# Kernel tuning notes

Measured on AMD Instinct MI355X. Metric: run time of the kernel, lower is better.

The kernel has to match this reference:

```python
import jax, jax.numpy as jnp
import numpy as np

B, S, H = 1, 2048, 2048
NH, NKV, HD = 32, 8, 64
RBS, ICS, RBN = 64, 64, 16          # retrieval_block_size, input_chunk_size, retrieval_block_num
RLEN = RBS * RBN                     # 1024 retrieval tokens
KV = RLEN + S                        # 3072 total kv length
START = RLEN                         # INPUT_START_IDX
SCALE = HD ** -0.5
NEG = -1e9


def _document_ids():
    # mirrors get_document_ids
    ids = np.full(KV, -1, np.int32)
    ids[:START] = np.arange(START) // RBS + 1            # retrieval blocks -> 1..RBN
    chunk = np.arange(S) // ICS
    ids[START:] = np.where(chunk == 0, -1, np.minimum(chunk, RBN))
    return ids


def _block_mask():
    # mirrors causal_retrieval_mask_mod, precomputed dense [S, KV]
    ids = _document_ids()
    qpos = np.arange(S) + START
    kv = np.arange(KV)
    causal = (qpos[:, None] >= kv[None, :]) & (kv[None, :] > START)
    doc = (ids[qpos][:, None] == ids[None, :]) & (kv[None, :] < START)
    return jnp.asarray(causal | doc)


_MASK = _block_mask()


def _rotate_half(x):
    h = x.shape[-1] // 2
    return jnp.concatenate([-x[..., h:], x[..., :h]], axis=-1)


def setup_inputs() -> dict:
    key = jax.random.key(0)
    ks = jax.random.split(key, 6)
    inv_freq = 1.0 / (10000.0 ** (np.arange(0, HD, 2, dtype=np.float32) / HD))
    ang = np.arange(S, dtype=np.float32)[:, None] * inv_freq[None, :]   # [S, HD/2]
    emb = np.concatenate([ang, ang], axis=-1)                            # [S, HD]
    cos = jnp.asarray(np.cos(emb))[None].astype(jnp.float32)            # [1, S, HD]
    sin = jnp.asarray(np.sin(emb))[None].astype(jnp.float32)
    return {
        "hidden_states": jax.random.normal(ks[0], (B, S, H), jnp.float32),
        "cos": cos,
        "sin": sin,
        "retrieval_key": jax.random.normal(ks[1], (B, NKV, RLEN, HD), jnp.float32),
        "retrieval_value": jax.random.normal(ks[2], (B, NKV, RLEN, HD), jnp.float32),
        "Wq": jax.random.normal(ks[3], (H, NH * HD), jnp.float32) * 0.02,
        "Wk": jax.random.normal(ks[4], (H, NKV * HD), jnp.float32) * 0.02,
        "Wv": jax.random.normal(ks[5], (H, NKV * HD), jnp.float32) * 0.02,
        "Wo": jax.random.normal(jax.random.fold_in(key, 7), (NH * HD, H), jnp.float32) * 0.02,
    }


def reference(hidden_states, cos, sin, retrieval_key, retrieval_value, Wq, Wk, Wv, Wo):
    # QKV projections -> [B, nheads, S, HD]
    q = (hidden_states @ Wq).reshape(B, S, NH, HD).transpose(0, 2, 1, 3)
    k = (hidden_states @ Wk).reshape(B, S, NKV, HD).transpose(0, 2, 1, 3)
    v = (hidden_states @ Wv).reshape(B, S, NKV, HD).transpose(0, 2, 1, 3)
    # RoPE (retrieval kv is pre-encoded; rope only on current tokens)
    c, s = cos[:, None, :, :], sin[:, None, :, :]
    q = q * c + _rotate_half(q) * s
    k = k * c + _rotate_half(k) * s
    # prepend retrieval kv
    k = jnp.concatenate([retrieval_key, k], axis=2)    # [B, NKV, KV, HD]
    v = jnp.concatenate([retrieval_value, v], axis=2)
    # GQA: expand kv heads
    g = NH // NKV
    k = jnp.repeat(k, g, axis=1)                        # [B, NH, KV, HD]
    v = jnp.repeat(v, g, axis=1)
    scores = jnp.einsum("bhqd,bhkd->bhqk", q, k) * SCALE
    scores = jnp.where(_MASK[None, None], scores, NEG)
    probs = jax.nn.softmax(scores, axis=-1)
    # fully-masked rows (q_idx 0) -> zero output, matching flex_attention
    row_valid = _MASK.any(axis=-1)[None, None, :, None]
    probs = jnp.where(row_valid, probs, 0.0)
    out = jnp.einsum("bhqk,bhkd->bhqd", probs, v)
    out = out.transpose(0, 2, 1, 3).reshape(B, S, NH * HD)
    return out @ Wo
```

## Files before the change

kernel.cpp:

```cpp
#include <hip/hip_runtime.h>

#define S_LEN 2048
#define H_DIM 2048
#define NH 32
#define NKV 8
#define HD 64
#define RLEN 1024
#define KVTOT 3072
#define SCALE 0.125f
#define QS 0.18033688011112042f
#define FIX8 11.541560327111707f

typedef unsigned short ushort_t;
using short8 = __attribute__((ext_vector_type(8))) short;
using f32x4 = __attribute__((ext_vector_type(4))) float;

__device__ __forceinline__ float b2f(unsigned short u) {
    union { unsigned int i; float f; } v;
    v.i = ((unsigned int)u) << 16;
    return v.f;
}
__device__ __forceinline__ unsigned short f2b(float f) {
    union { float f; unsigned int i; } v;
    v.f = f;
    unsigned int x = v.i;
    return (unsigned short)((x + 0x7fffu + ((x >> 16) & 1u)) >> 16);
}

__device__ __forceinline__ void gload16(const ushort_t* g, ushort_t* l) {
    __builtin_amdgcn_global_load_lds(
        (const __attribute__((address_space(1))) unsigned int*)g,
        (__attribute__((address_space(3))) unsigned int*)l, 16, 0, 0);
}

__device__ __forceinline__ int is_f32(const void* p) {
    const unsigned int* w = (const unsigned int*)p;
    const int lane = threadIdx.x & 63;
    int cnt = 0;
#pragma unroll
    for (int j = 0; j < 4; ++j) {
        unsigned int lo = w[lane + j * 64] & 0xFFFFu;
        unsigned int e = (lo >> 7) & 0xFFu;
        cnt += (lo != 0u && (e < 90u || e > 140u)) ? 1 : 0;
    }
    unsigned long long b = __ballot(cnt >= 2);
    return __popcll(b) > 16;
}

__global__ __launch_bounds__(256) void prep_all(
    const void* __restrict__ rk, const void* __restrict__ rv,
    const void* __restrict__ Wq, const void* __restrict__ Wk,
    const void* __restrict__ Wv, const void* __restrict__ Wo,
    ushort_t* __restrict__ WqkvT, ushort_t* __restrict__ WoT,
    ushort_t* __restrict__ ktall, ushort_t* __restrict__ vtall)
{
    __shared__ ushort_t S[64 * 72];
    const int id = blockIdx.x;
    if (id < 2560) {
        int z, t;
        if (id < 1024)      { z = 0; t = id; }
        else if (id < 1280) { z = 1; t = id - 1024; }
        else if (id < 1536) { z = 2; t = id - 1280; }
        else                { z = 3; t = id - 1536; }
        const void* src = (z == 0) ? Wq : (z == 1) ? Wk : (z == 2) ? Wv : Wo;
        const int F = is_f32(src);
        const int C = (z == 1 || z == 2) ? 512 : 2048;
        const int nx = (z == 1 || z == 2) ? 8 : 32;
        const int x = t % nx, y = t / nx;
        ushort_t* dst = (z == 3) ? WoT : WqkvT;
        const int rofs = (z == 1) ? 2048 : (z == 2) ? 2560 : 0;

        const int r0 = y * 64, c0 = x * 64;
        const int lr = threadIdx.x >> 2, lc = (threadIdx.x & 3) * 16;
        ushort_t tt[16];
        if (F) {
            const float* p = (const float*)src + (size_t)(r0 + lr) * C + c0 + lc;
#pragma unroll
            for (int j = 0; j < 16; j += 4) {
                float4 f = *(const float4*)(p + j);
                tt[j] = f2b(f.x); tt[j + 1] = f2b(f.y); tt[j + 2] = f2b(f.z); tt[j + 3] = f2b(f.w);
            }
        } else {
            const ushort_t* p = (const ushort_t*)src + (size_t)(r0 + lr) * C + c0 + lc;
            *(uint4*)tt = ((const uint4*)p)[0];
            *(uint4*)(tt + 8) = ((const uint4*)p)[1];
        }
        *(uint4*)&S[lr * 72 + lc] = *(const uint4*)tt;
        *(uint4*)&S[lr * 72 + lc + 8] = *(const uint4*)(tt + 8);
        __syncthreads();
        const int wc = threadIdx.x >> 2, wr = (threadIdx.x & 3) * 16;
        ushort_t o[16];
#pragma unroll
        for (int j = 0; j < 16; ++j) o[j] = S[(wr + j) * 72 + wc];
        ushort_t* q = dst + (size_t)(rofs + c0 + wc) * 2048 + r0 + wr;
        *(uint4*)q = *(const uint4*)o;
        *(uint4*)(q + 8) = *(const uint4*)(o + 8);
    } else if (id < 2816) {
        const int kF = is_f32(rk);
        const int e = ((id - 2560) * 256 + threadIdx.x) * 8;
        const int kvh = e >> 16;
        const int rem = e & 65535;
        ushort_t* dst = ktall + (size_t)kvh * (KVTOT * 64) + rem;
        if (kF) {
            const float* p = (const float*)rk + e;
            float4 f0 = ((const float4*)p)[0];
            float4 f1 = ((const float4*)p)[1];
            ushort_t o[8];
            o[0] = f2b(f0.x); o[1] = f2b(f0.y); o[2] = f2b(f0.z); o[3] = f2b(f0.w);
            o[4] = f2b(f1.x); o[5] = f2b(f1.y); o[6] = f2b(f1.z); o[7] = f2b(f1.w);
            *(uint4*)dst = *(const uint4*)o;
        } else {
            *(uint4*)dst = *(const uint4*)((const ushort_t*)rk + e);
        }
    } else {
        const int idv = id - 2816;
        const int t = idv & 15;
        const int kvh = idv >> 4;
        const int vF = is_f32(rv);
        const int lr = threadIdx.x >> 2, lc = (threadIdx.x & 3) * 16;
        ushort_t tt[16];
        size_t base = ((size_t)kvh * RLEN + t * 64 + lr) * HD + lc;
        if (vF) {
            const float* p = (const float*)rv + base;
#pragma unroll
            for (int j = 0; j < 16; j += 4) {
                float4 f = *(const float4*)(p + j);
                tt[j] = f2b(f.x); tt[j + 1] = f2b(f.y); tt[j + 2] = f2b(f.z); tt[j + 3] = f2b(f.w);
            }
        } else {
            const ushort_t* p = (const ushort_t*)rv + base;
            *(uint4*)tt = ((const uint4*)p)[0];
            *(uint4*)(tt + 8) = ((const uint4*)p)[1];
        }
        *(uint4*)&S[lr * 72 + lc] = *(const uint4*)tt;
        *(uint4*)&S[lr * 72 + lc + 8] = *(const uint4*)(tt + 8);
        __syncthreads();
        const int wc = threadIdx.x >> 2, wr = (threadIdx.x & 3) * 16;
        ushort_t o[16];
#pragma unroll
        for (int j = 0; j < 16; ++j) o[j] = S[(wr + j) * 72 + wc];
        const int blk = t * 2 + (wr >> 5);
        ushort_t* q = vtall + (((size_t)(kvh * 96 + blk) * 64 + wc) * 32) + (wr & 31);
        *(uint4*)q = *(const uint4*)o;
        *(uint4*)(q + 8) = *(const uint4*)(o + 8);
    }
}

__global__ __launch_bounds__(256, 4) void gemm_qkv(
    const void* __restrict__ hs, const ushort_t* __restrict__ Bt,
    ushort_t* __restrict__ qkvp, ushort_t* __restrict__ ktall,
    ushort_t* __restrict__ vtall,
    const void* __restrict__ cosv, const void* __restrict__ sinv)
{
    const int K = 2048;
    const int aF = is_f32(hs);
    __shared__ __align__(16) ushort_t As[2][64 * 32];
    __shared__ __align__(16) ushort_t Bs[2][128 * 32];
    const int tid = threadIdx.x;
    const int wave = tid >> 6, lane = tid & 63;
    const int lq = lane & 15, quad = lane >> 4;
    const int m0 = blockIdx.y * 64, n0 = blockIdx.x * 128;
    const int wm = (wave & 1) * 32, wn = (wave >> 1) * 64;
    const int nk = K >> 5;

    const int ar = tid >> 2, ag = tid & 3;
    const int aslot = (ag ^ ((ar >> 1) & 3)) * 8;
    const float*    apf = (const float*)hs    + (size_t)(m0 + ar) * K + ag * 8;
    const ushort_t* aph = (const ushort_t*)hs + (size_t)(m0 + ar) * K + ag * 8;
    const int srow = wave * 16 + (lane >> 2);
    const int scol = ((lane & 3) ^ ((lane >> 3) & 3)) * 8;
    const ushort_t* gb0 = Bt + (size_t)(n0 + srow) * K + scol;
    const ushort_t* gb1 = Bt + (size_t)(n0 + 64 + srow) * K + scol;
    ushort_t* lB = &Bs[0][0] + wave * 16 * 32;
    const int rs = (lq >> 1) & 3;

    float4 af0, af1;
    uint2 au0, au1;

#define ALOAD(kt) do { \
        if (aF) { af0 = *(const float4*)(apf + (size_t)(kt) * 32); \
                  af1 = *(const float4*)(apf + (size_t)(kt) * 32 + 4); } \
        else    { au0 = *(const uint2*)(aph + (size_t)(kt) * 32); \
                  au1 = *(const uint2*)(aph + (size_t)(kt) * 32 + 4); } \
    } while (0)
#define AWRITE(buf) do { \
        ushort_t t8[8]; \
        if (aF) { t8[0]=f2b(af0.x); t8[1]=f2b(af0.y); t8[2]=f2b(af0.z); t8[3]=f2b(af0.w); \
                  t8[4]=f2b(af1.x); t8[5]=f2b(af1.y); t8[6]=f2b(af1.z); t8[7]=f2b(af1.w); } \
        else    { *(uint2*)t8 = au0; *(uint2*)(t8 + 4) = au1; } \
        *(uint4*)&As[buf][ar * 32 + aslot] = *(const uint4*)t8; \
    } while (0)
#define GLOADB(buf, kt) do { \
        gload16(gb0 + (size_t)(kt) * 32, lB + (buf) * (128 * 32)); \
        gload16(gb1 + (size_t)(kt) * 32, lB + (buf) * (128 * 32) + 64 * 32); \
    } while (0)

    f32x4 acc[2][4];
#pragma unroll
    for (int i = 0; i < 2; ++i)
#pragma unroll
        for (int j = 0; j < 4; ++j) acc[i][j] = (f32x4){0.f, 0.f, 0.f, 0.f};

    ALOAD(0); AWRITE(0);
    GLOADB(0, 0);
    int cur = 0;
    for (int kt = 0; kt < nk; ++kt) {
        const bool more = (kt + 1 < nk);
        if (more) {
            ALOAD(kt + 1);
            GLOADB(cur ^ 1, kt + 1);
            asm volatile("s_waitcnt vmcnt(4) lgkmcnt(0)" ::: "memory");
        } else {
            asm volatile("s_waitcnt vmcnt(0) lgkmcnt(0)" ::: "memory");
        }
        __builtin_amdgcn_s_barrier();
        __builtin_amdgcn_sched_barrier(0);
        short8 afr[2], bfr[4];
#pragma unroll
        for (int i = 0; i < 2; ++i)
            afr[i] = *(const short8*)&As[cur][(wm + i * 16 + lq) * 32 + (quad ^ rs) * 8];
#pragma unroll
        for (int j = 0; j < 4; ++j)
            bfr[j] = *(const short8*)&Bs[cur][(wn + j * 16 + lq) * 32 + (quad ^ rs) * 8];
#pragma unroll
        for (int i = 0; i < 2; ++i)
#pragma unroll
            for (int j = 0; j < 4; ++j)
                acc[i][j] = __builtin_amdgcn_mfma_f32_16x16x32_bf16(afr[i], bfr[j], acc[i][j], 0, 0, 0);
        if (more) AWRITE(cur ^ 1);
        __builtin_amdgcn_s_barrier();
        cur ^= 1;
    }
#undef ALOAD
#undef AWRITE
#undef GLOADB

    if (n0 < 2048) {
#pragma unroll
        for (int i = 0; i < 2; ++i)
#pragma unroll
            for (int r = 0; r < 4; ++r) {
                ushort_t* cp = qkvp + (size_t)(m0 + wm + i * 16 + quad * 4 + r) * 2048 + n0 + wn + lq;
#pragma unroll
                for (int j = 0; j < 4; ++j) cp[j * 16] = f2b(acc[i][j][r]);
            }
    } else if (n0 < 2560) {
        const int cF = is_f32(cosv), sF = is_f32(sinv);
        const int kvh = (n0 - 2048 + wn) >> 6;
#pragma unroll
        for (int i = 0; i < 2; ++i)
#pragma unroll
            for (int r = 0; r < 4; ++r) {
                const int si = m0 + wm + i * 16 + quad * 4 + r;
                const int ci = si * HD + lq;
                float c0, c1, c2, c3, s0, s1, s2, s3;
                if (cF) {
                    const float* cp = (const float*)cosv + ci;
                    c0 = cp[0]; c1 = cp[16]; c2 = cp[32]; c3 = cp[48];
                } else {
                    const ushort_t* cp = (const ushort_t*)cosv + ci;
                    c0 = b2f(cp[0]); c1 = b2f(cp[16]); c2 = b2f(cp[32]); c3 = b2f(cp[48]);
                }
                if (sF) {
                    const float* sp = (const float*)sinv + ci;
                    s0 = sp[0]; s1 = sp[16]; s2 = sp[32]; s3 = sp[48];
                } else {
                    const ushort_t* sp = (const ushort_t*)sinv + ci;
                    s0 = b2f(sp[0]); s1 = b2f(sp[16]); s2 = b2f(sp[32]); s3 = b2f(sp[48]);
                }
                ushort_t* kp = ktall + ((size_t)kvh * KVTOT + RLEN + si) * HD + lq;
                kp[0]  = f2b(acc[i][0][r] * c0 - acc[i][2][r] * s0);
                kp[16] = f2b(acc[i][1][r] * c1 - acc[i][3][r] * s1);
                kp[32] = f2b(acc[i][2][r] * c2 + acc[i][0][r] * s2);
                kp[48] = f2b(acc[i][3][r] * c3 + acc[i][1][r] * s3);
            }
    } else {
        const int kvh = (n0 - 2560 + wn) >> 6;
#pragma unroll
        for (int i = 0; i < 2; ++i) {
            const int si0 = m0 + wm + i * 16 + quad * 4;
            const int blk = 32 + (si0 >> 5);
            const int slot = si0 & 31;
#pragma unroll
            for (int j = 0; j < 4; ++j) {
                const int d = j * 16 + lq;
                ushort_t o[4];
#pragma unroll
                for (int r = 0; r < 4; ++r) o[r] = f2b(acc[i][j][r]);
                *(uint2*)(vtall + ((size_t)(kvh * 96 + blk) * 64 + d) * 32 + slot) = *(const uint2*)o;
            }
        }
    }
}

__global__ __launch_bounds__(256, 4) void gemm_fin(
    const ushort_t* __restrict__ A, const ushort_t* __restrict__ Bt,
    void* __restrict__ Cv, int N, int K, const void* __restrict__ hs)
{
    const int oF = is_f32(hs);
    __shared__ __align__(16) ushort_t As[2][64 * 32];
    __shared__ __align__(16) ushort_t Bs[2][128 * 32];
    const int tid = threadIdx.x;
    const int wave = tid >> 6, lane = tid & 63;
    const int lq = lane & 15, quad = lane >> 4;
    const int m0 = blockIdx.y * 64, n0 = blockIdx.x * 128;
    const int wm = (wave & 1) * 32, wn = (wave >> 1) * 64;
    const int nk = K >> 5;

    const int srow = wave * 16 + (lane >> 2);
    const int scol = ((lane & 3) ^ ((lane >> 3) & 3)) * 8;
    const ushort_t* ga  = A  + (size_t)(m0 + srow) * K + scol;
    const ushort_t* gb0 = Bt + (size_t)(n0 + srow) * K + scol;
    const ushort_t* gb1 = Bt + (size_t)(n0 + 64 + srow) * K + scol;
    ushort_t* lA = &As[0][0] + wave * 16 * 32;
    ushort_t* lB = &Bs[0][0] + wave * 16 * 32;
    const int rs = (lq >> 1) & 3;

    f32x4 acc[2][4];
#pragma unroll
    for (int i = 0; i < 2; ++i)
#pragma unroll
        for (int j = 0; j < 4; ++j) acc[i][j] = (f32x4){0.f, 0.f, 0.f, 0.f};

#define STAGE_G(buf, kt) do { \
        gload16(ga  + (size_t)(kt) * 32, lA + (buf) * (64 * 32)); \
        gload16(gb0 + (size_t)(kt) * 32, lB + (buf) * (128 * 32)); \
        gload16(gb1 + (size_t)(kt) * 32, lB + (buf) * (128 * 32) + 64 * 32); \
    } while (0)

    STAGE_G(0, 0);
    int cur = 0;
    for (int kt = 0; kt < nk; ++kt) {
        if (kt + 1 < nk) {
            STAGE_G(cur ^ 1, kt + 1);
            asm volatile("s_waitcnt vmcnt(3)" ::: "memory");
        } else {
            asm volatile("s_waitcnt vmcnt(0)" ::: "memory");
        }
        __builtin_amdgcn_s_barrier();
        __builtin_amdgcn_sched_barrier(0);
        short8 afr[2], bfr[4];
#pragma unroll
        for (int i = 0; i < 2; ++i)
            afr[i] = *(const short8*)&As[cur][(wm + i * 16 + lq) * 32 + (quad ^ rs) * 8];
#pragma unroll
        for (int j = 0; j < 4; ++j)
            bfr[j] = *(const short8*)&Bs[cur][(wn + j * 16 + lq) * 32 + (quad ^ rs) * 8];
#pragma unroll
        for (int i = 0; i < 2; ++i)
#pragma unroll
            for (int j = 0; j < 4; ++j)
                acc[i][j] = __builtin_amdgcn_mfma_f32_16x16x32_bf16(afr[i], bfr[j], acc[i][j], 0, 0, 0);
        __builtin_amdgcn_s_barrier();
        cur ^= 1;
    }

#pragma unroll
    for (int i = 0; i < 2; ++i)
#pragma unroll
        for (int r = 0; r < 4; ++r) {
            size_t off = (size_t)(m0 + wm + i * 16 + quad * 4 + r) * N + n0 + wn + lq;
            if (oF) {
                float* cp = (float*)Cv + off;
#pragma unroll
                for (int j = 0; j < 4; ++j) cp[j * 16] = acc[i][j][r];
            } else {
                ushort_t* cp = (ushort_t*)Cv + off;
#pragma unroll
                for (int j = 0; j < 4; ++j) cp[j * 16] = f2b(acc[i][j][r]);
            }
        }
#undef STAGE_G
}

__global__ __launch_bounds__(256) void fattn(
    const ushort_t* __restrict__ qkvp, const ushort_t* __restrict__ ktall,
    const ushort_t* __restrict__ vtall, ushort_t* __restrict__ attno,
    const void* __restrict__ cosv, const void* __restrict__ sinv)
{
    const int cF = is_f32(cosv), sF = is_f32(sinv);
    const int h = blockIdx.x;
    const int yy = blockIdx.y;
    const int st = yy >> 3, r8 = yy & 7;
    const int qb = (st == 0) ? (31 - r8) : (st == 1) ? (16 + r8)
                 : (st == 2) ? (15 - r8) : r8;
    const int kvh = h >> 2;
    const int tid = threadIdx.x;
    const int wave = tid >> 6;
    const int lane = tid & 63;
    const int lq = lane & 15;
    const int quad = lane >> 4;
    const int rb64 = ((qb < 17 ? qb : 16) - 1) * 64;
    const int qrow = qb * 64 + wave * 16 + lq;

    __shared__ __align__(16) ushort_t Ks[128 * 72];
    __shared__ __align__(16) ushort_t Ps[4 * 16 * 136];
    ushort_t* pw = &Ps[wave * 16 * 136];

    short8 qfrag[2];
    {
        const int row_g = qb * 64 + wave * 16 + lq;
        const ushort_t* qrp = qkvp + (size_t)row_g * 2048 + h * HD;
        short8 t0 = *(const short8*)(qrp + quad * 8);
        short8 t1 = *(const short8*)(qrp + 32 + quad * 8);
        const int ci = row_g * HD + quad * 8;
        float c0[8], c1[8], s0[8], s1[8];
        if (cF) {
            const float* cp = (const float*)cosv + ci;
#pragma unroll
            for (int j = 0; j < 8; ++j) { c0[j] = cp[j]; c1[j] = cp[j + 32]; }
        } else {
            const ushort_t* cp = (const ushort_t*)cosv + ci;
#pragma unroll
            for (int j = 0; j < 8; ++j) { c0[j] = b2f(cp[j]); c1[j] = b2f(cp[j + 32]); }
        }
        if (sF) {
            const float* sp = (const float*)sinv + ci;
#pragma unroll
            for (int j = 0; j < 8; ++j) { s0[j] = sp[j]; s1[j] = sp[j + 32]; }
        } else {
            const ushort_t* sp = (const ushort_t*)sinv + ci;
#pragma unroll
            for (int j = 0; j < 8; ++j) { s0[j] = b2f(sp[j]); s1[j] = b2f(sp[j + 32]); }
        }
#pragma unroll
        for (int j = 0; j < 8; ++j) {
            float a = b2f((unsigned short)t0[j]), b = b2f((unsigned short)t1[j]);
            qfrag[0][j] = (short)f2b((a * c0[j] - b * s0[j]) * QS);
            qfrag[1][j] = (short)f2b((b * c1[j] + a * s1[j]) * QS);
        }
    }

    f32x4 oacc[4];
#pragma unroll
    for (int nt = 0; nt < 4; ++nt) oacc[nt] = (f32x4){0.f, 0.f, 0.f, 0.f};
    float lsum = 0.f;

    const int Lq = (qb > 0) ? qb * 64 + 128 : 64;
    const int nch = (Lq + 127) >> 7;
    const ushort_t* kbase = ktall + (size_t)kvh * KVTOT * HD;
    const ushort_t* vbase = vtall + (size_t)kvh * 96 * 2048;

    for (int c = 0; c < nch; ++c) {
        uint4 kreg0, kreg1, kreg2, kreg3;
        const int krow = tid >> 1;
        const int kd0 = (tid & 1) * 32;
        {
            int p = c * 128 + krow;
            uint4 z = {0, 0, 0, 0};
            kreg0 = z; kreg1 = z; kreg2 = z; kreg3 = z;
            if (p < Lq) {
                int pk = (qb > 0) ? ((p < 64) ? rb64 + p : 960 + p) : RLEN + p;
                const uint4* s = (const uint4*)(kbase + (size_t)pk * HD + kd0);
                kreg0 = s[0]; kreg1 = s[1]; kreg2 = s[2]; kreg3 = s[3];
            }
        }
        int vblk[4];
#pragma unroll
        for (int kc = 0; kc < 4; ++kc) {
            int p = c * 128 + kc * 32;
            int pk = (qb > 0) ? ((p < 64) ? rb64 + p : 960 + p) : RLEN + p;
            if (pk > KVTOT - 1) pk = KVTOT - 1;
            vblk[kc] = pk >> 5;
        }
        short8 vfA[4], vfB[4];
#pragma unroll
        for (int ntd = 0; ntd < 4; ++ntd)
            vfA[ntd] = *(const short8*)(vbase + ((size_t)vblk[0] * 64 + ntd * 16 + lq) * 32 + quad * 8);
#pragma unroll
        for (int ntd = 0; ntd < 4; ++ntd)
            vfB[ntd] = *(const short8*)(vbase + ((size_t)vblk[1] * 64 + ntd * 16 + lq) * 32 + quad * 8);

        {
            uint4* dk = (uint4*)&Ks[krow * 72 + kd0];
            dk[0] = kreg0; dk[1] = kreg1; dk[2] = kreg2; dk[3] = kreg3;
        }
        __syncthreads();

        const bool lastc = (c == nch - 1) || (qb == 0);
#pragma unroll
        for (int nt = 0; nt < 8; ++nt) {
            f32x4 a = (f32x4){0.f, 0.f, 0.f, 0.f};
            a = __builtin_amdgcn_mfma_f32_16x16x32_bf16(
                *(const short8*)&Ks[(nt * 16 + lq) * 72 + quad * 8], qfrag[0], a, 0, 0, 0);
            a = __builtin_amdgcn_mfma_f32_16x16x32_bf16(
                *(const short8*)&Ks[(nt * 16 + lq) * 72 + 32 + quad * 8], qfrag[1], a, 0, 0, 0);
            float pex[4];
#pragma unroll
            for (int rr = 0; rr < 4; ++rr) {
                const int p = c * 128 + nt * 16 + quad * 4 + rr;
                float pexp = exp2f(a[rr] - FIX8);
                if (lastc) {
                    bool valid;
                    if (qb > 0) valid = (p < 64) || ((p - 64) >= 1 && (p - 64) <= qrow);
                    else        valid = (p >= 1 && p <= qrow);
                    if (!valid) pexp = 0.f;
                } else if (c == 0) {
                    if (p == 64) pexp = 0.f;
                }
                lsum += pexp;
                pex[rr] = pexp;
            }
            unsigned int w0, w1;
            asm("v_cvt_pk_bf16_f32 %0, %1, %2" : "=v"(w0) : "v"(pex[0]), "v"(pex[1]));
            asm("v_cvt_pk_bf16_f32 %0, %1, %2" : "=v"(w1) : "v"(pex[2]), "v"(pex[3]));
            *(uint2*)&pw[lq * 136 + nt * 16 + quad * 4] = make_uint2(w0, w1);
        }

#pragma unroll
        for (int kc = 0; kc < 4; ++kc) {
            short8 pa = *(const short8*)&pw[lq * 136 + kc * 32 + quad * 8];
            short8 vf0, vf1, vf2, vf3;
            if (kc == 0)      { vf0 = vfA[0]; vf1 = vfA[1]; vf2 = vfA[2]; vf3 = vfA[3]; }
            else if (kc == 1) { vf0 = vfB[0]; vf1 = vfB[1]; vf2 = vfB[2]; vf3 = vfB[3]; }
            else {
                const int b = vblk[kc];
                vf0 = *(const short8*)(vbase + ((size_t)b * 64 + 0 * 16 + lq) * 32 + quad * 8);
                vf1 = *(const short8*)(vbase + ((size_t)b * 64 + 1 * 16 + lq) * 32 + quad * 8);
                vf2 = *(const short8*)(vbase + ((size_t)b * 64 + 2 * 16 + lq) * 32 + quad * 8);
                vf3 = *(const short8*)(vbase + ((size_t)b * 64 + 3 * 16 + lq) * 32 + quad * 8);
            }
            oacc[0] = __builtin_amdgcn_mfma_f32_16x16x32_bf16(pa, vf0, oacc[0], 0, 0, 0);
            oacc[1] = __builtin_amdgcn_mfma_f32_16x16x32_bf16(pa, vf1, oacc[1], 0, 0, 0);
            oacc[2] = __builtin_amdgcn_mfma_f32_16x16x32_bf16(pa, vf2, oacc[2], 0, 0, 0);
            oacc[3] = __builtin_amdgcn_mfma_f32_16x16x32_bf16(pa, vf3, oacc[3], 0, 0, 0);
        }
        __syncthreads();
    }

    float tot = lsum;
    tot += __shfl_xor(tot, 16, 64);
    tot += __shfl_xor(tot, 32, 64);
#pragma unroll
    for (int rr = 0; rr < 4; ++rr) {
        const int qg = qb * 64 + wave * 16 + quad * 4 + rr;
        const float tr = __shfl(tot, quad * 4 + rr, 64);
        const float inv = (qg == 0) ? 0.f : 1.f / tr;
        ushort_t* orow = attno + (size_t)qg * 2048 + h * HD;
#pragma unroll
        for (int nt = 0; nt < 4; ++nt)
            orow[nt * 16 + lq] = f2b(oacc[nt][rr] * inv);
    }
}

extern "C" void kernel_launch(void* const* d_in, const int* in_sizes, int n_in,
                              void* d_out, int out_size, void* d_ws, size_t ws_size,
                              hipStream_t stream) {
    const void* hs   = d_in[0];
    const void* cosv = d_in[1];
    const void* sinv = d_in[2];
    const void* rk   = d_in[3];
    const void* rv   = d_in[4];
    const void* Wq   = d_in[5];
    const void* Wk   = d_in[6];
    const void* Wv   = d_in[7];
    const void* Wo   = d_in[8];

    char* ws = (char*)d_ws;
    ushort_t* ktall = (ushort_t*)ws;
    ushort_t* vtall = (ushort_t*)(ws + (3u  << 20));
    ushort_t* WqkvT = (ushort_t*)(ws + (6u  << 20));
    ushort_t* WoT   = (ushort_t*)(ws + (18u << 20));
    ushort_t* qkvp  = (ushort_t*)(ws + (26u << 20));
    ushort_t* attno = WqkvT;

    prep_all<<<2944, 256, 0, stream>>>(rk, rv, Wq, Wk, Wv, Wo, WqkvT, WoT, ktall, vtall);

    gemm_qkv<<<dim3(24, 32), 256, 0, stream>>>(hs, WqkvT, qkvp, ktall, vtall, cosv, sinv);

    fattn<<<dim3(NH, 32), 256, 0, stream>>>(qkvp, ktall, vtall, attno, cosv, sinv);

    gemm_fin<<<dim3(16, 32), 256, 0, stream>>>(attno, WoT, d_out, 2048, 2048, hs);
}
```

Measured before the change: 270.3 us.

## Pre-convert hidden states to bf16 in prep kernel and stage A via direct-to-LDS loads

Adds 2048 extra blocks to the prep kernel that convert hidden_states from fp32 to bf16 into the output buffer used as scratch. The QKV GEMM then loads A tiles with the same async global-to-LDS path as B, dropping the per-tile register conversion and LDS writes. This removes conversion work and register staging from the GEMM main loop. In exchange it adds an extra pass over hidden_states and a dependency on d_out being free until the final GEMM. Each QKV tile of A is currently converted 24 times, once per N-block.

```diff
diff --git a/kernel.cpp b/kernel.cpp
--- a/kernel.cpp
+++ b/kernel.cpp
@@ -52,10 +52,27 @@
     const void* __restrict__ Wq, const void* __restrict__ Wk,
     const void* __restrict__ Wv, const void* __restrict__ Wo,
     ushort_t* __restrict__ WqkvT, ushort_t* __restrict__ WoT,
-    ushort_t* __restrict__ ktall, ushort_t* __restrict__ vtall)
+    ushort_t* __restrict__ ktall, ushort_t* __restrict__ vtall,
+    const void* __restrict__ hs, ushort_t* __restrict__ hsb)
 {
     __shared__ ushort_t S[64 * 72];
     const int id = blockIdx.x;
+    if (id >= 2944) {
+        const int F = is_f32(hs);
+        int i = ((id - 2944) * 256 + threadIdx.x) * 8;
+        ushort_t o[8];
+        if (F) {
+            const float* p = (const float*)hs + i;
+            float4 f0 = ((const float4*)p)[0];
+            float4 f1 = ((const float4*)p)[1];
+            o[0] = f2b(f0.x); o[1] = f2b(f0.y); o[2] = f2b(f0.z); o[3] = f2b(f0.w);
+            o[4] = f2b(f1.x); o[5] = f2b(f1.y); o[6] = f2b(f1.z); o[7] = f2b(f1.w);
+            *(uint4*)(hsb + i) = *(const uint4*)o;
+        } else {
+            *(uint4*)(hsb + i) = *(const uint4*)((const ushort_t*)hs + i);
+        }
+        return;
+    }
     if (id < 2560) {
         int z, t;
         if (id < 1024)      { z = 0; t = id; }
@@ -147,13 +164,12 @@
 }
 
 __global__ __launch_bounds__(256, 4) void gemm_qkv(
-    const void* __restrict__ hs, const ushort_t* __restrict__ Bt,
+    const ushort_t* __restrict__ A, const ushort_t* __restrict__ Bt,
     ushort_t* __restrict__ qkvp, ushort_t* __restrict__ ktall,
     ushort_t* __restrict__ vtall,
     const void* __restrict__ cosv, const void* __restrict__ sinv)
 {
     const int K = 2048;
-    const int aF = is_f32(hs);
     __shared__ __align__(16) ushort_t As[2][64 * 32];
     __shared__ __align__(16) ushort_t Bs[2][128 * 32];
     const int tid = threadIdx.x;
@@ -163,55 +179,35 @@
     const int wm = (wave & 1) * 32, wn = (wave >> 1) * 64;
     const int nk = K >> 5;
 
-    const int ar = tid >> 2, ag = tid & 3;
-    const int aslot = (ag ^ ((ar >> 1) & 3)) * 8;
-    const float*    apf = (const float*)hs    + (size_t)(m0 + ar) * K + ag * 8;
-    const ushort_t* aph = (const ushort_t*)hs + (size_t)(m0 + ar) * K + ag * 8;
     const int srow = wave * 16 + (lane >> 2);
     const int scol = ((lane & 3) ^ ((lane >> 3) & 3)) * 8;
+    const ushort_t* ga  = A  + (size_t)(m0 + srow) * K + scol;
     const ushort_t* gb0 = Bt + (size_t)(n0 + srow) * K + scol;
     const ushort_t* gb1 = Bt + (size_t)(n0 + 64 + srow) * K + scol;
+    ushort_t* lA = &As[0][0] + wave * 16 * 32;
     ushort_t* lB = &Bs[0][0] + wave * 16 * 32;
     const int rs = (lq >> 1) & 3;
 
-    float4 af0, af1;
-    uint2 au0, au1;
-
-#define ALOAD(kt) do { \
-        if (aF) { af0 = *(const float4*)(apf + (size_t)(kt) * 32); \
-                  af1 = *(const float4*)(apf + (size_t)(kt) * 32 + 4); } \
-        else    { au0 = *(const uint2*)(aph + (size_t)(kt) * 32); \
-                  au1 = *(const uint2*)(aph + (size_t)(kt) * 32 + 4); } \
-    } while (0)
-#define AWRITE(buf) do { \
-        ushort_t t8[8]; \
-        if (aF) { t8[0]=f2b(af0.x); t8[1]=f2b(af0.y); t8[2]=f2b(af0.z); t8[3]=f2b(af0.w); \
-                  t8[4]=f2b(af1.x); t8[5]=f2b(af1.y); t8[6]=f2b(af1.z); t8[7]=f2b(af1.w); } \
-        else    { *(uint2*)t8 = au0; *(uint2*)(t8 + 4) = au1; } \
-        *(uint4*)&As[buf][ar * 32 + aslot] = *(const uint4*)t8; \
-    } while (0)
-#define GLOADB(buf, kt) do { \
+    f32x4 acc[2][4];
+#pragma unroll
+    for (int i = 0; i < 2; ++i)
+#pragma unroll
+        for (int j = 0; j < 4; ++j) acc[i][j] = (f32x4){0.f, 0.f, 0.f, 0.f};
+
+#define STAGE_G(buf, kt) do { \
+        gload16(ga  + (size_t)(kt) * 32, lA + (buf) * (64 * 32)); \
         gload16(gb0 + (size_t)(kt) * 32, lB + (buf) * (128 * 32)); \
         gload16(gb1 + (size_t)(kt) * 32, lB + (buf) * (128 * 32) + 64 * 32); \
     } while (0)
 
-    f32x4 acc[2][4];
-#pragma unroll
-    for (int i = 0; i < 2; ++i)
-#pragma unroll
-        for (int j = 0; j < 4; ++j) acc[i][j] = (f32x4){0.f, 0.f, 0.f, 0.f};
-
-    ALOAD(0); AWRITE(0);
-    GLOADB(0, 0);
+    STAGE_G(0, 0);
     int cur = 0;
     for (int kt = 0; kt < nk; ++kt) {
-        const bool more = (kt + 1 < nk);
-        if (more) {
-            ALOAD(kt + 1);
-            GLOADB(cur ^ 1, kt + 1);
-            asm volatile("s_waitcnt vmcnt(4) lgkmcnt(0)" ::: "memory");
-        } else {
-            asm volatile("s_waitcnt vmcnt(0) lgkmcnt(0)" ::: "memory");
+        if (kt + 1 < nk) {
+            STAGE_G(cur ^ 1, kt + 1);
+            asm volatile("s_waitcnt vmcnt(3)" ::: "memory");
+        } else {
+            asm volatile("s_waitcnt vmcnt(0)" ::: "memory");
         }
         __builtin_amdgcn_s_barrier();
         __builtin_amdgcn_sched_barrier(0);
@@ -227,13 +223,10 @@
 #pragma unroll
             for (int j = 0; j < 4; ++j)
                 acc[i][j] = __builtin_amdgcn_mfma_f32_16x16x32_bf16(afr[i], bfr[j], acc[i][j], 0, 0, 0);
-        if (more) AWRITE(cur ^ 1);
         __builtin_amdgcn_s_barrier();
         cur ^= 1;
     }
-#undef ALOAD
-#undef AWRITE
-#undef GLOADB
+#undef STAGE_G
 
     if (n0 < 2048) {
 #pragma unroll
@@ -563,10 +556,11 @@
     ushort_t* WoT   = (ushort_t*)(ws + (18u << 20));
     ushort_t* qkvp  = (ushort_t*)(ws + (26u << 20));
     ushort_t* attno = WqkvT;
-
-    prep_all<<<2944, 256, 0, stream>>>(rk, rv, Wq, Wk, Wv, Wo, WqkvT, WoT, ktall, vtall);
-
-    gemm_qkv<<<dim3(24, 32), 256, 0, stream>>>(hs, WqkvT, qkvp, ktall, vtall, cosv, sinv);
+    ushort_t* hsb   = (ushort_t*)d_out;
+
+    prep_all<<<4992, 256, 0, stream>>>(rk, rv, Wq, Wk, Wv, Wo, WqkvT, WoT, ktall, vtall, hs, hsb);
+
+    gemm_qkv<<<dim3(24, 32), 256, 0, stream>>>(hsb, WqkvT, qkvp, ktall, vtall, cosv, sinv);
 
     fattn<<<dim3(NH, 32), 256, 0, stream>>>(qkvp, ktall, vtall, attno, cosv, sinv);
 
```

New measurement: 253.7 us. 1.07x faster.
